# Performance work log

Measured on AMD Instinct MI355X. Metric: run time of the kernel, lower is better.

Reference implementation:

```python
import jax, jax.numpy as jnp
import numpy as np

B, C, N, T, Hd, L, F = 128, 8, 256, 64, 256, 2, 32  # batch, conv_channels, num_nodes(=hidden), obs_len, hidden, num_layers, filter_num


def setup_inputs() -> dict:
    key = jax.random.key(0)
    ks = jax.random.split(key, 20)
    s = 0.05
    f32 = jnp.float32
    return {
        "x": jax.random.normal(ks[0], (B, C, N, T), f32),
        "wst": jax.random.normal(ks[1], (C,), f32) * s,            # st_conv 1x1 weight
        "bst": jax.random.normal(ks[2], (1,), f32) * s,
        "Wh": jax.random.normal(ks[3], (Hd, N), f32) * s,           # hidden Linear
        "bh": jax.random.normal(ks[4], (Hd,), f32) * s,
        "Wih": jax.random.normal(ks[5], (4 * Hd, Hd), f32) * s,     # LSTM
        "Whh": jax.random.normal(ks[6], (4 * Hd, Hd), f32) * s,
        "bih": jax.random.normal(ks[7], (4 * Hd,), f32) * s,
        "bhh": jax.random.normal(ks[8], (4 * Hd,), f32) * s,
        "Wd": jax.random.normal(ks[9], (Hd, 2 * Hd), f32) * s,      # den Linear(2h->h)
        "bd": jax.random.normal(ks[10], (Hd,), f32) * s,
        "Wc": jax.random.normal(ks[11], (F, T), f32) * s,           # attention conv kernel (filter_num,1,obs_len,1) squeezed
        "bc": jax.random.normal(ks[12], (F,), f32) * s,
        "Wl1": jax.random.normal(ks[13], (F, 2 * Hd), f32) * s,     # attention linear1
        "bl1": jax.random.normal(ks[14], (F,), f32) * s,
        "Wl2": jax.random.normal(ks[15], (Hd, 2 * Hd + F), f32) * s,  # attention linear2
        "bl2": jax.random.normal(ks[16], (Hd,), f32) * s,
        "wend": jax.random.normal(ks[17], (C,), f32) * s,           # end_conv 1x1 weight
        "bend": jax.random.normal(ks[18], (C,), f32) * s,
    }


def _forward(x, wst, bst, Wh, bh, Wih, Whh, bih, bhh, Wd, bd, Wc, bc, Wl1, bl1, Wl2, bl2, wend, bend):
    b = x.shape[0]
    # st_conv (1x1 over channels) + relu, then (B, obs_len, num_nodes)
    y = jax.nn.relu(jnp.einsum("bcnt,c->bnt", x, wst) + bst[0])
    xcon = jax.nn.relu(jnp.einsum("bnt,hn->bth", y, Wh) + bh)  # (B, T, Hd)

    def lstm_cell(xt, ht, ct):
        g = xt @ Wih.T + bih + ht @ Whh.T + bhh
        i, f, gg, o = jnp.split(g, 4, axis=1)
        c2 = jax.nn.sigmoid(f) * ct + jax.nn.sigmoid(i) * jnp.tanh(gg)
        h2 = jax.nn.sigmoid(o) * jnp.tanh(c2)
        return h2, c2

    def attention(Hbuf, htt2):
        # Hbuf: (b, T, Hd); htt2: (b, 2Hd)
        w = htt2 @ Wl1.T + bl1                                   # (b, F)
        cv = jax.nn.relu(jnp.einsum("bto,ft->bof", Hbuf, Wc) + bc)  # (b, Hd, F)
        alpha = jax.nn.sigmoid(jnp.sum(cv * w[:, None, :], axis=2))  # (b, Hd)
        v = jnp.sum(alpha[:, :, None] * cv, axis=1)              # (b, F)
        return jax.nn.relu(jnp.concatenate([htt2, v], axis=1)) @ Wl2.T + bl2

    def step(carry, xt):
        ht, ct, attn_out, Hbuf = carry
        xi = xt
        new_ht = attn_out
        for _ in range(L):
            xd = jnp.concatenate([xi, attn_out], axis=1) @ Wd.T + bd
            ht, ct = lstm_cell(xd, ht, ct)
            htt2 = jnp.concatenate([ct, ht], axis=1)             # (b, 2Hd)
            new_ht = attention(Hbuf, htt2)                       # (b, Hd)
            output = jnp.concatenate([ht, new_ht], axis=1) @ Wd.T + bd
            Hbuf = jax.nn.relu(jnp.concatenate([Hbuf[:, 1:, :], output[:, None, :]], axis=1))
            attn_out = new_ht
            xi = output
        return (ht, ct, attn_out, Hbuf), new_ht

    z = jnp.zeros((b, Hd), x.dtype)
    carry0 = (z, z, z, jnp.zeros((b, T, Hd), x.dtype))
    _, res = jax.lax.scan(step, carry0, jnp.transpose(xcon, (1, 0, 2)))  # (T, b, Hd)
    r = jax.nn.relu(jnp.transpose(res, (1, 2, 0)))              # (b, Hd, T)
    # end_conv 1x1: (b, C, Hd, T)
    return r[:, None, :, :] * wend[None, :, None, None] + bend[None, :, None, None]


def reference(x, wst, bst, Wh, bh, Wih, Whh, bih, bhh, Wd, bd, Wc, bc, Wl1, bl1, Wl2, bl2, wend, bend):
    return _forward(x, wst, bst, Wh, bh, Wih, Whh, bih, bhh, Wd, bd, Wc, bc, Wl1, bl1, Wl2, bl2, wend, bend)
```

## Files before the change

kernel.cpp:

```cpp
#include <hip/hip_runtime.h>
#include <hip/hip_bf16.h>

typedef unsigned int uint;
typedef unsigned short ushort;
typedef __fp16 half2_t __attribute__((ext_vector_type(2)));

__device__ __forceinline__ ushort f16b(float x){
  return __builtin_bit_cast(ushort, (_Float16)x);
}
__device__ __forceinline__ uint pk_rne(float a, float b){
  return (uint)f16b(a) | ((uint)f16b(b) << 16);
}
__device__ __forceinline__ void pk_hl(float a, float b, uint& h, uint& l){
  _Float16 ha = (_Float16)a, hb = (_Float16)b;
  float la = (a - (float)ha) * 2048.f;
  float lb = (b - (float)hb) * 2048.f;
  h = (uint)__builtin_bit_cast(ushort, ha) | ((uint)__builtin_bit_cast(ushort, hb) << 16);
  l = pk_rne(la, lb);
}
__device__ __forceinline__ float fdot2(uint a, uint b, float c){
#if __has_builtin(__builtin_amdgcn_fdot2)
  return __builtin_amdgcn_fdot2(__builtin_bit_cast(half2_t, a),
                                __builtin_bit_cast(half2_t, b), c, false);
#else
  half2_t ha = __builtin_bit_cast(half2_t, a), hb = __builtin_bit_cast(half2_t, b);
  return c + (float)ha.x*(float)hb.x + (float)ha.y*(float)hb.y;
#endif
}
__device__ __forceinline__ float f16sel(uint p, uint hi){
  ushort us = hi ? (ushort)(p >> 16) : (ushort)(p & 0xffffu);
  return (float)__builtin_bit_cast(_Float16, us);
}
__device__ __forceinline__ float sigm(float x){ return 1.0f/(1.0f+__expf(-x)); }
__device__ __forceinline__ float tanh_(float x){
  x = fminf(fmaxf(x, -15.f), 15.f);
  float e = __expf(-2.f*x);
  return (1.f-e)/(1.f+e);
}
#define LO_SCALE (1.0f/2048.0f)


__global__ void kPack(const float* __restrict__ Wd, const float* __restrict__ Wih,
                      const float* __restrict__ Whh, const float* __restrict__ Wl1,
                      const float* __restrict__ Wl2, const float* __restrict__ Wc,
                      const float* __restrict__ Wh,  const float* __restrict__ bih,
                      const float* __restrict__ bhh,
                      uint4* __restrict__ Wd4, uint4* __restrict__ Wc4hi,
                      uint4* __restrict__ Wc4lo, uint4* __restrict__ Wl24,
                      float* __restrict__ Wl1f, uint* __restrict__ Wcrot,
                      uint* __restrict__ WhT2, float* __restrict__ bcomb)
{
  const int NTOT = 32768 + 65536 + 34816 + 16384 + 65536 + 32768 + 1024;
  for (int idx = blockIdx.x*blockDim.x + threadIdx.x; idx < NTOT; idx += gridDim.x*blockDim.x){
    int i = idx;
    if (i < 32768){
      int kpp=i>>8, o=i&255, k0=4*kpp;
      uint h0,l0,h1,l1;
      pk_hl(Wd[o*512+k0],   Wd[o*512+k0+1], h0,l0);
      pk_hl(Wd[o*512+k0+2], Wd[o*512+k0+3], h1,l1);
      Wd4[i] = make_uint4(h0,l0,h1,l1); continue; }
    i -= 32768;
    if (i < 65536){
      int kp=i>>8, hh=i&255;
      uint wh[4], wl[4];
      #pragma unroll
      for (int gi=0; gi<4; gi++){
        int row = gi*256+hh;
        float a,b;
        if (kp<128){ a=Wih[row*256+2*kp]; b=Wih[row*256+2*kp+1]; }
        else       { a=Whh[row*256+2*(kp-128)]; b=Whh[row*256+2*(kp-128)+1]; }
        pk_hl(a,b,wh[gi],wl[gi]);
      }
      Wc4hi[i] = make_uint4(wh[0],wh[1],wh[2],wh[3]);
      Wc4lo[i] = make_uint4(wl[0],wl[1],wl[2],wl[3]); continue; }
    i -= 65536;
    if (i < 34816){
      int kpp=i>>8, o=i&255, k0=4*kpp;
      uint h0,l0,h1,l1;
      pk_hl(Wl2[o*544+k0],   Wl2[o*544+k0+1], h0,l0);
      pk_hl(Wl2[o*544+k0+2], Wl2[o*544+k0+3], h1,l1);
      Wl24[i] = make_uint4(h0,l0,h1,l1); continue; }
    i -= 34816;
    if (i < 16384){ int kk=i>>5, f=i&31; Wl1f[i] = Wl1[f*512+kk]; continue; }
    i -= 16384;
    if (i < 65536){ int bb=i>>10, r=i&1023, ps=r>>5, f=r&31;
      float lo = Wc[f*64 + ((2*ps   - bb) & 63)];
      float hi = Wc[f*64 + ((2*ps+1 - bb) & 63)];
      Wcrot[i] = pk_rne(lo, hi); continue; }
    i -= 65536;
    if (i < 32768){ int np=i>>8, h=i&255;
      WhT2[i] = pk_rne(Wh[h*256+2*np], Wh[h*256+2*np+1]); continue; }
    i -= 32768;
    bcomb[i] = bih[i] + bhh[i];
  }
}

__global__ void k1a(const float* __restrict__ x, const float* __restrict__ wst,
                    const float* __restrict__ bst, ushort* __restrict__ yT)
{
  int b = blockIdx.x, tq = blockIdx.y, n = threadIdx.x;
  float acc[16];
  #pragma unroll
  for (int k=0;k<16;k++) acc[k]=0.f;
  for (int c=0;c<8;c++){
    const float4* xp = (const float4*)(x + ((size_t)((b*8+c)*256 + n)*64 + tq*16));
    float wc = wst[c];
    #pragma unroll
    for (int q=0;q<4;q++){
      float4 v = xp[q];
      acc[4*q+0] += v.x*wc; acc[4*q+1] += v.y*wc;
      acc[4*q+2] += v.z*wc; acc[4*q+3] += v.w*wc;
    }
  }
  float b0 = bst[0];
  #pragma unroll
  for (int k=0;k<16;k++){
    float v = fmaxf(acc[k]+b0, 0.f);
    yT[(size_t)(b*64 + tq*16 + k)*256 + n] = f16b(v);
  }
}

__global__ void k1b(const uint* __restrict__ yT2, const uint* __restrict__ WhT2,
                    const float* __restrict__ bh, float* __restrict__ xcon)
{
  __shared__ uint yp[8192];
  int b = blockIdx.x, tid = threadIdx.x;
  for (int i = tid; i < 8192; i += 256) yp[i] = yT2[(size_t)b*8192 + i];
  __syncthreads();
  int h = tid;
  float bias = bh[h];
  for (int tq=0;tq<4;tq++){
    float acc[16];
    #pragma unroll
    for (int k=0;k<16;k++) acc[k]=0.f;
    for (int np=0;np<128;np++){
      uint w2 = WhT2[np*256 + h];
      #pragma unroll
      for (int k=0;k<16;k++)
        acc[k] = fdot2(yp[(tq*16+k)*128 + np], w2, acc[k]);
    }
    #pragma unroll
    for (int k=0;k<16;k++)
      xcon[(size_t)(b*64 + tq*16 + k)*256 + h] = fmaxf(acc[k]+bias, 0.f);
  }
}

__global__ __launch_bounds__(1024, 1)
void TPALSTM_17205638987874_kernel(const float* __restrict__ xcon,
        const uint4* __restrict__ Wd4, const uint4* __restrict__ Wc4hi,
        const uint4* __restrict__ Wc4lo, const uint4* __restrict__ Wl24,
        const float* __restrict__ Wl1f, const uint* __restrict__ Wcrot,
        const float* __restrict__ bd, const float* __restrict__ bcomb,
        const float* __restrict__ bl1, const float* __restrict__ bl2,
        const float* __restrict__ bc, float* __restrict__ res)
{
  __shared__ uint  Hp[32][256];
  __shared__ uint  cvp[256][17];
  __shared__ float gp[16][256];
  __shared__ float p4[4][256];
  __shared__ float ht[256], ct[256], alpha[256];
  __shared__ __align__(16) uint2 APR2[288];
  __shared__ uint  wpair[16];

  int b = blockIdx.x, tid = threadIdx.x;
  int g = tid >> 8, o = tid & 255;

  for (int i = tid; i < 32*256; i += 1024) ((uint*)Hp)[i] = 0u;
  if (tid < 256){ ht[tid]=0.f; ct[tid]=0.f; }
  if (tid >= 128 && tid < 256) APR2[tid] = make_uint2(0u,0u);
  __syncthreads();

  int base = 0;
  for (int t=0;t<64;t++){
    if (tid < 128){
      const float* xr = xcon + (size_t)(b*64+t)*256;
      uint h,l; pk_hl(xr[2*tid], xr[2*tid+1], h, l);
      APR2[tid] = make_uint2(h,l);
    }
    __syncthreads();

    for (int l=0;l<2;l++){
      {
        float ahi=0.f, alo=0.f;
        const uint4* wp = Wd4 + (size_t)(g*32)*256 + o;
        const uint4* ap = (const uint4*)(APR2 + g*64);
        #pragma unroll 4
        for (int kpp=0;kpp<32;kpp++){
          uint4 w = wp[0]; wp += 256;
          uint4 A = ap[kpp];
          ahi = fdot2(A.x, w.x, ahi); alo = fdot2(A.y, w.x, alo); alo = fdot2(A.x, w.y, alo);
          ahi = fdot2(A.z, w.z, ahi); alo = fdot2(A.w, w.z, alo); alo = fdot2(A.z, w.w, alo);
        }
        p4[g][o] = ahi + alo*LO_SCALE;
      }
      __syncthreads();
      if (tid < 128){
        int o0=2*tid, o1=o0+1;
        float x0 = p4[0][o0]+p4[1][o0]+p4[2][o0]+p4[3][o0]+bd[o0];
        float x1 = p4[0][o1]+p4[1][o1]+p4[2][o1]+p4[3][o1]+bd[o1];
        uint h,l; pk_hl(x0,x1,h,l); APR2[tid]=make_uint2(h,l);
      } else if (tid < 256){
        int j=tid-128; uint h,l; pk_hl(ht[2*j], ht[2*j+1], h, l); APR2[tid]=make_uint2(h,l);
      }
      __syncthreads();
      {
        float ih=0.f,il=0.f,fh=0.f,fl=0.f,gh=0.f,gl=0.f,oh=0.f,ol=0.f;
        const uint4* whp = Wc4hi + (size_t)(g*64)*256 + o;
        const uint4* wlp = Wc4lo + (size_t)(g*64)*256 + o;
        #pragma unroll 2
        for (int kp=g*64; kp<g*64+64; kp++){
          uint4 w = whp[0]; whp += 256;
          uint4 v = wlp[0]; wlp += 256;
          uint2 A = APR2[kp];
          ih=fdot2(A.x,w.x,ih); il=fdot2(A.y,w.x,il); il=fdot2(A.x,v.x,il);
          fh=fdot2(A.x,w.y,fh); fl=fdot2(A.y,w.y,fl); fl=fdot2(A.x,v.y,fl);
          gh=fdot2(A.x,w.z,gh); gl=fdot2(A.y,w.z,gl); gl=fdot2(A.x,v.z,gl);
          oh=fdot2(A.x,w.w,oh); ol=fdot2(A.y,w.w,ol); ol=fdot2(A.x,v.w,ol);
        }
        gp[g*4+0][o]=ih+il*LO_SCALE; gp[g*4+1][o]=fh+fl*LO_SCALE;
        gp[g*4+2][o]=gh+gl*LO_SCALE; gp[g*4+3][o]=oh+ol*LO_SCALE;
      }
      __syncthreads();
      if (g==0){
        float gi = sigm (gp[0][o]+gp[4][o]+gp[8][o] +gp[12][o]+bcomb[o]);
        float gf = sigm (gp[1][o]+gp[5][o]+gp[9][o] +gp[13][o]+bcomb[256+o]);
        float gg = tanh_(gp[2][o]+gp[6][o]+gp[10][o]+gp[14][o]+bcomb[512+o]);
        float go = sigm (gp[3][o]+gp[7][o]+gp[11][o]+gp[15][o]+bcomb[768+o]);
        float c2 = gf*ct[o] + gi*gg;
        float h2 = go*tanh_(c2);
        ct[o]=c2; ht[o]=h2;
      }
      __syncthreads();
      if (tid < 128){ uint h,l; pk_hl(fmaxf(ct[2*tid],0.f), fmaxf(ct[2*tid+1],0.f), h,l); APR2[tid]=make_uint2(h,l); }
      else if (tid < 256){ int j=tid-128; uint h,l; pk_hl(fmaxf(ht[2*j],0.f), fmaxf(ht[2*j+1],0.f), h,l); APR2[tid]=make_uint2(h,l); }
      if (g==2 && o < 32){
        int f = o;
        float a=0.f;
        const float* w = Wl1f + f;
        for (int k=0;k<256;k++) a += ct[k]*w[k*32];
        for (int k=0;k<256;k++) a += ht[k]*w[(256+k)*32];
        float wtot = a + bl1[f];
        float wn = __shfl_xor(wtot,1);
        if (!(f&1)) wpair[f>>1] = pk_rne(wtot,wn);
      }
      if (g < 2){
        int rb = base & 63;
        const uint* wr = Wcrot + rb*1024 + g*16;
        float acc[16];
        #pragma unroll
        for (int j=0;j<16;j++) acc[j]=0.f;
        for (int ps=0;ps<32;ps++){
          uint hp = Hp[ps][o];
          const uint* w = wr + ps*32;
          #pragma unroll
          for (int j=0;j<16;j++) acc[j] = fdot2(hp, w[j], acc[j]);
        }
        #pragma unroll
        for (int jj=0;jj<8;jj++){
          int f0 = g*16 + 2*jj;
          cvp[o][g*8+jj] = pk_rne(fmaxf(acc[2*jj]+bc[f0],0.f),
                                  fmaxf(acc[2*jj+1]+bc[f0+1],0.f));
        }
      }
      __syncthreads();
      if (tid < 256){
        float s=0.f;
        #pragma unroll
        for (int p=0;p<16;p++) s = fdot2(cvp[tid][p], wpair[p], s);
        alpha[tid] = sigm(s);
      }
      __syncthreads();
      {
        int og = tid>>5, f = tid&31;
        uint hi = f&1; int fp=f>>1;
        float s=0.f;
        #pragma unroll
        for (int oo=0;oo<8;oo++){
          int oa = og*8+oo;
          s += alpha[oa]*f16sel(cvp[oa][fp], hi);
        }
        ((float*)gp)[og*32+f] = s;
      }
      __syncthreads();
      if (tid<32){
        float v=0.f;
        #pragma unroll
        for (int q=0;q<32;q++) v += ((float*)gp)[q*32+tid];
        float vn = __shfl_xor(v,1);
        if (!(tid&1)){
          uint h,l; pk_hl(fmaxf(v,0.f), fmaxf(vn,0.f), h,l);
          APR2[256+(tid>>1)]=make_uint2(h,l);
        }
      }
      __syncthreads();
      {
        float ahi=0.f, alo=0.f;
        const uint4* wp = Wl24 + (size_t)(g*34)*256 + o;
        const uint4* ap = (const uint4*)(APR2 + g*68);
        #pragma unroll 4
        for (int kpp=0;kpp<34;kpp++){
          uint4 w = wp[0]; wp += 256;
          uint4 A = ap[kpp];
          ahi = fdot2(A.x, w.x, ahi); alo = fdot2(A.y, w.x, alo); alo = fdot2(A.x, w.y, alo);
          ahi = fdot2(A.z, w.z, ahi); alo = fdot2(A.w, w.z, alo); alo = fdot2(A.z, w.w, alo);
        }
        p4[g][o] = ahi + alo*LO_SCALE;
      }
      __syncthreads();
      if (tid<128){ uint h,l; pk_hl(ht[2*tid], ht[2*tid+1], h,l); APR2[tid]=make_uint2(h,l); }
      else if (tid<256){
        int j=tid-128, o0=2*j, o1=o0+1;
        float n0 = p4[0][o0]+p4[1][o0]+p4[2][o0]+p4[3][o0]+bl2[o0];
        float n1 = p4[0][o1]+p4[1][o1]+p4[2][o1]+p4[3][o1]+bl2[o1];
        uint h,l; pk_hl(n0,n1,h,l); APR2[tid]=make_uint2(h,l);
        if (l==1){}
        if (1){
        }
        p4[0][o0] = n0; p4[0][o1] = n1;
      }
      __syncthreads();
      if (l==1 && tid>=128 && tid<256){
        int j=tid-128, o0=2*j, o1=o0+1;
        float* rr = res + (size_t)(t*128+b)*256;
        rr[o0] = p4[0][o0]; rr[o1] = p4[0][o1];
      }
      {
        float ahi=0.f, alo=0.f;
        const uint4* wp = Wd4 + (size_t)(g*32)*256 + o;
        const uint4* ap = (const uint4*)(APR2 + g*64);
        #pragma unroll 4
        for (int kpp=0;kpp<32;kpp++){
          uint4 w = wp[0]; wp += 256;
          uint4 A = ap[kpp];
          ahi = fdot2(A.x, w.x, ahi); alo = fdot2(A.y, w.x, alo); alo = fdot2(A.x, w.y, alo);
          ahi = fdot2(A.z, w.z, ahi); alo = fdot2(A.w, w.z, alo); alo = fdot2(A.z, w.w, alo);
        }
        __syncthreads();
        p4[g][o] = ahi + alo*LO_SCALE;
      }
      __syncthreads();
      if (tid<128){
        int o0=2*tid, o1=o0+1;
        float u0 = p4[0][o0]+p4[1][o0]+p4[2][o0]+p4[3][o0]+bd[o0];
        float u1 = p4[0][o1]+p4[1][o1]+p4[2][o1]+p4[3][o1]+bd[o1];
        uint h,l; pk_hl(u0, u1, h, l);
        APR2[tid]=make_uint2(h,l);
        int s = base & 63, ps = s>>1; uint hb = (uint)(s&1);
        uint h0 = (uint)f16b(fmaxf(u0,0.f)), h1 = (uint)f16b(fmaxf(u1,0.f));
        uint old0 = Hp[ps][o0], old1 = Hp[ps][o1];
        Hp[ps][o0] = hb ? ((old0&0xFFFFu)|(h0<<16)) : ((old0&0xFFFF0000u)|h0);
        Hp[ps][o1] = hb ? ((old1&0xFFFFu)|(h1<<16)) : ((old1&0xFFFF0000u)|h1);
      }
      __syncthreads();
      base++;
    }
  }
}

__global__ void k3(const float* __restrict__ res, const float* __restrict__ wend,
                   const float* __restrict__ bend, float* __restrict__ out)
{
  __shared__ float r2[64][257];
  int b = blockIdx.x, tid = threadIdx.x;
  for (int i = tid; i < 16384; i += 256){
    int t = i >> 8, h = i & 255;
    r2[t][h] = fmaxf(res[(size_t)(t*128+b)*256 + h], 0.f);
  }
  __syncthreads();
  int tt = tid & 63, hg = tid >> 6;
  for (int c=0;c<8;c++){
    float we = wend[c], be = bend[c];
    for (int hh=0;hh<64;hh++){
      int h = hg*64 + hh;
      out[((size_t)(b*8+c)*256 + h)*64 + tt] = r2[tt][h]*we + be;
    }
  }
}

extern "C" __attribute__((visibility("default"), used))
void kernel_launch(void* const* d_in, const int* in_sizes, int n_in,
                   void* d_out, int out_size, void* d_ws, size_t ws_size,
                   hipStream_t stream)
{
  const float* x    = (const float*)d_in[0];
  const float* wst  = (const float*)d_in[1];
  const float* bst  = (const float*)d_in[2];
  const float* Wh   = (const float*)d_in[3];
  const float* bh   = (const float*)d_in[4];
  const float* Wih  = (const float*)d_in[5];
  const float* Whh  = (const float*)d_in[6];
  const float* bih  = (const float*)d_in[7];
  const float* bhh  = (const float*)d_in[8];
  const float* Wd   = (const float*)d_in[9];
  const float* bd   = (const float*)d_in[10];
  const float* Wc   = (const float*)d_in[11];
  const float* bc   = (const float*)d_in[12];
  const float* Wl1  = (const float*)d_in[13];
  const float* bl1  = (const float*)d_in[14];
  const float* Wl2  = (const float*)d_in[15];
  const float* bl2  = (const float*)d_in[16];
  const float* wend = (const float*)d_in[17];
  const float* bend = (const float*)d_in[18];

  char* ws = (char*)d_ws;
  uint4* Wd4   = (uint4*)(ws + 0);
  uint4* Wc4hi = (uint4*)(ws + 524288);
  uint4* Wc4lo = (uint4*)(ws + 1572864);
  uint4* Wl24  = (uint4*)(ws + 2621440);
  float* Wl1f  = (float*)(ws + 3178496);
  uint*  Wcrot = (uint*) (ws + 3244032);
  uint*  WhT2  = (uint*) (ws + 3506176);
  float* bcomb = (float*)(ws + 3637248);
  ushort* yT   = (ushort*)(ws + 3641344);
  float* xcon  = (float*)(ws + 7835648);
  float* res   = (float*)(ws + 16224256);

  kPack<<<512, 256, 0, stream>>>(Wd, Wih, Whh, Wl1, Wl2, Wc, Wh, bih, bhh,
                                 Wd4, Wc4hi, Wc4lo, Wl24, Wl1f, Wcrot, WhT2, bcomb);
  k1a<<<dim3(128,4), 256, 0, stream>>>(x, wst, bst, yT);
  k1b<<<128, 256, 0, stream>>>((const uint*)yT, WhT2, bh, xcon);
  TPALSTM_17205638987874_kernel<<<128, 1024, 0, stream>>>(xcon, Wd4, Wc4hi, Wc4lo, Wl24,
                                                          Wl1f, Wcrot, bd, bcomb, bl1, bl2, bc, res);
  k3<<<128, 256, 0, stream>>>(res, wend, bend, (float*)d_out);
}
```

Before: 5.108 ms.

## Use hi/lo split fp16 for attention conv and spread it over all wave groups

The attention convolution now stores the history buffer and the rotated conv weights as a hi/lo fp16 pair and does three fdot2 per pair, which should give close to fp32 accuracy. The conv values are kept in fp32 shared memory rather than packed fp16. The conv work moves from two thread groups of 16 filters each to all four groups of 8 filters, and the Wl1 projection moves to group 3. This adds LDS traffic and extra dot products for accuracy, partly offset by the better spread of work across groups.

```diff
diff --git a/kernel.cpp b/kernel.cpp
--- a/kernel.cpp
+++ b/kernel.cpp
@@ -27,10 +27,6 @@
   return c + (float)ha.x*(float)hb.x + (float)ha.y*(float)hb.y;
 #endif
 }
-__device__ __forceinline__ float f16sel(uint p, uint hi){
-  ushort us = hi ? (ushort)(p >> 16) : (ushort)(p & 0xffffu);
-  return (float)__builtin_bit_cast(_Float16, us);
-}
 __device__ __forceinline__ float sigm(float x){ return 1.0f/(1.0f+__expf(-x)); }
 __device__ __forceinline__ float tanh_(float x){
   x = fminf(fmaxf(x, -15.f), 15.f);
@@ -47,8 +43,9 @@
                       const float* __restrict__ bhh,
                       uint4* __restrict__ Wd4, uint4* __restrict__ Wc4hi,
                       uint4* __restrict__ Wc4lo, uint4* __restrict__ Wl24,
-                      float* __restrict__ Wl1f, uint* __restrict__ Wcrot,
-                      uint* __restrict__ WhT2, float* __restrict__ bcomb)
+                      float* __restrict__ Wl1f, uint* __restrict__ WcrotH,
+                      uint* __restrict__ WcrotL, uint* __restrict__ WhT2,
+                      float* __restrict__ bcomb)
 {
   const int NTOT = 32768 + 65536 + 34816 + 16384 + 65536 + 32768 + 1024;
   for (int idx = blockIdx.x*blockDim.x + threadIdx.x; idx < NTOT; idx += gridDim.x*blockDim.x){
@@ -84,9 +81,10 @@
     if (i < 16384){ int kk=i>>5, f=i&31; Wl1f[i] = Wl1[f*512+kk]; continue; }
     i -= 16384;
     if (i < 65536){ int bb=i>>10, r=i&1023, ps=r>>5, f=r&31;
-      float lo = Wc[f*64 + ((2*ps   - bb) & 63)];
-      float hi = Wc[f*64 + ((2*ps+1 - bb) & 63)];
-      Wcrot[i] = pk_rne(lo, hi); continue; }
+      float va = Wc[f*64 + ((2*ps   - bb) & 63)];
+      float vb = Wc[f*64 + ((2*ps+1 - bb) & 63)];
+      uint h,l; pk_hl(va, vb, h, l);
+      WcrotH[i] = h; WcrotL[i] = l; continue; }
     i -= 65536;
     if (i < 32768){ int np=i>>8, h=i&255;
       WhT2[i] = pk_rne(Wh[h*256+2*np], Wh[h*256+2*np+1]); continue; }
@@ -149,23 +147,25 @@
 void TPALSTM_17205638987874_kernel(const float* __restrict__ xcon,
         const uint4* __restrict__ Wd4, const uint4* __restrict__ Wc4hi,
         const uint4* __restrict__ Wc4lo, const uint4* __restrict__ Wl24,
-        const float* __restrict__ Wl1f, const uint* __restrict__ Wcrot,
+        const float* __restrict__ Wl1f, const uint* __restrict__ WcrotH,
+        const uint* __restrict__ WcrotL,
         const float* __restrict__ bd, const float* __restrict__ bcomb,
         const float* __restrict__ bl1, const float* __restrict__ bl2,
         const float* __restrict__ bc, float* __restrict__ res)
 {
-  __shared__ uint  Hp[32][256];
-  __shared__ uint  cvp[256][17];
+  __shared__ uint  HpH[32][256];
+  __shared__ uint  HpL[32][256];
+  __shared__ float cvs[256][33];
   __shared__ float gp[16][256];
   __shared__ float p4[4][256];
   __shared__ float ht[256], ct[256], alpha[256];
   __shared__ __align__(16) uint2 APR2[288];
-  __shared__ uint  wpair[16];
+  __shared__ float wv[32];
 
   int b = blockIdx.x, tid = threadIdx.x;
   int g = tid >> 8, o = tid & 255;
 
-  for (int i = tid; i < 32*256; i += 1024) ((uint*)Hp)[i] = 0u;
+  for (int i = tid; i < 8192; i += 1024){ ((uint*)HpH)[i] = 0u; ((uint*)HpL)[i] = 0u; }
   if (tid < 256){ ht[tid]=0.f; ct[tid]=0.f; }
   if (tid >= 128 && tid < 256) APR2[tid] = make_uint2(0u,0u);
   __syncthreads();
@@ -233,51 +233,53 @@
       __syncthreads();
       if (tid < 128){ uint h,l; pk_hl(fmaxf(ct[2*tid],0.f), fmaxf(ct[2*tid+1],0.f), h,l); APR2[tid]=make_uint2(h,l); }
       else if (tid < 256){ int j=tid-128; uint h,l; pk_hl(fmaxf(ht[2*j],0.f), fmaxf(ht[2*j+1],0.f), h,l); APR2[tid]=make_uint2(h,l); }
-      if (g==2 && o < 32){
+      {
+        int rb = base & 63;
+        const uint* wrH = WcrotH + rb*1024 + g*8;
+        const uint* wrL = WcrotL + rb*1024 + g*8;
+        float ah[8], al[8];
+        #pragma unroll
+        for (int j=0;j<8;j++){ ah[j]=0.f; al[j]=0.f; }
+        for (int ps=0;ps<32;ps++){
+          uint hH = HpH[ps][o], hL = HpL[ps][o];
+          const uint* wH = wrH + ps*32;
+          const uint* wL = wrL + ps*32;
+          #pragma unroll
+          for (int j=0;j<8;j++){
+            ah[j] = fdot2(hH, wH[j], ah[j]);
+            al[j] = fdot2(hL, wH[j], al[j]);
+            al[j] = fdot2(hH, wL[j], al[j]);
+          }
+        }
+        #pragma unroll
+        for (int j=0;j<8;j++){
+          int f0 = g*8+j;
+          cvs[o][f0] = fmaxf(ah[j] + al[j]*LO_SCALE + bc[f0], 0.f);
+        }
+      }
+      if (g==3 && o < 32){
         int f = o;
         float a=0.f;
         const float* w = Wl1f + f;
         for (int k=0;k<256;k++) a += ct[k]*w[k*32];
         for (int k=0;k<256;k++) a += ht[k]*w[(256+k)*32];
-        float wtot = a + bl1[f];
-        float wn = __shfl_xor(wtot,1);
-        if (!(f&1)) wpair[f>>1] = pk_rne(wtot,wn);
-      }
-      if (g < 2){
-        int rb = base & 63;
-        const uint* wr = Wcrot + rb*1024 + g*16;
-        float acc[16];
-        #pragma unroll
-        for (int j=0;j<16;j++) acc[j]=0.f;
-        for (int ps=0;ps<32;ps++){
-          uint hp = Hp[ps][o];
-          const uint* w = wr + ps*32;
-          #pragma unroll
-          for (int j=0;j<16;j++) acc[j] = fdot2(hp, w[j], acc[j]);
-        }
-        #pragma unroll
-        for (int jj=0;jj<8;jj++){
-          int f0 = g*16 + 2*jj;
-          cvp[o][g*8+jj] = pk_rne(fmaxf(acc[2*jj]+bc[f0],0.f),
-                                  fmaxf(acc[2*jj+1]+bc[f0+1],0.f));
-        }
+        wv[f] = a + bl1[f];
       }
       __syncthreads();
       if (tid < 256){
         float s=0.f;
         #pragma unroll
-        for (int p=0;p<16;p++) s = fdot2(cvp[tid][p], wpair[p], s);
+        for (int f=0;f<32;f++) s += cvs[tid][f]*wv[f];
         alpha[tid] = sigm(s);
       }
       __syncthreads();
       {
         int og = tid>>5, f = tid&31;
-        uint hi = f&1; int fp=f>>1;
         float s=0.f;
         #pragma unroll
         for (int oo=0;oo<8;oo++){
           int oa = og*8+oo;
-          s += alpha[oa]*f16sel(cvp[oa][fp], hi);
+          s += alpha[oa]*cvs[oa][f];
         }
         ((float*)gp)[og*32+f] = s;
       }
@@ -313,9 +315,6 @@
         float n0 = p4[0][o0]+p4[1][o0]+p4[2][o0]+p4[3][o0]+bl2[o0];
         float n1 = p4[0][o1]+p4[1][o1]+p4[2][o1]+p4[3][o1]+bl2[o1];
         uint h,l; pk_hl(n0,n1,h,l); APR2[tid]=make_uint2(h,l);
-        if (l==1){}
-        if (1){
-        }
         p4[0][o0] = n0; p4[0][o1] = n1;
       }
       __syncthreads();
@@ -345,11 +344,19 @@
         float u1 = p4[0][o1]+p4[1][o1]+p4[2][o1]+p4[3][o1]+bd[o1];
         uint h,l; pk_hl(u0, u1, h, l);
         APR2[tid]=make_uint2(h,l);
+        float r0 = fmaxf(u0,0.f), r1 = fmaxf(u1,0.f);
+        _Float16 rh0 = (_Float16)r0, rh1 = (_Float16)r1;
+        uint h0 = (uint)__builtin_bit_cast(ushort, rh0);
+        uint h1 = (uint)__builtin_bit_cast(ushort, rh1);
+        uint l0 = (uint)f16b((r0-(float)rh0)*2048.f);
+        uint l1 = (uint)f16b((r1-(float)rh1)*2048.f);
         int s = base & 63, ps = s>>1; uint hb = (uint)(s&1);
-        uint h0 = (uint)f16b(fmaxf(u0,0.f)), h1 = (uint)f16b(fmaxf(u1,0.f));
-        uint old0 = Hp[ps][o0], old1 = Hp[ps][o1];
-        Hp[ps][o0] = hb ? ((old0&0xFFFFu)|(h0<<16)) : ((old0&0xFFFF0000u)|h0);
-        Hp[ps][o1] = hb ? ((old1&0xFFFFu)|(h1<<16)) : ((old1&0xFFFF0000u)|h1);
+        uint oldH0 = HpH[ps][o0], oldH1 = HpH[ps][o1];
+        uint oldL0 = HpL[ps][o0], oldL1 = HpL[ps][o1];
+        HpH[ps][o0] = hb ? ((oldH0&0xFFFFu)|(h0<<16)) : ((oldH0&0xFFFF0000u)|h0);
+        HpH[ps][o1] = hb ? ((oldH1&0xFFFFu)|(h1<<16)) : ((oldH1&0xFFFF0000u)|h1);
+        HpL[ps][o0] = hb ? ((oldL0&0xFFFFu)|(l0<<16)) : ((oldL0&0xFFFF0000u)|l0);
+        HpL[ps][o1] = hb ? ((oldL1&0xFFFFu)|(l1<<16)) : ((oldL1&0xFFFF0000u)|l1);
       }
       __syncthreads();
       base++;
@@ -403,23 +410,25 @@
   const float* bend = (const float*)d_in[18];
 
   char* ws = (char*)d_ws;
-  uint4* Wd4   = (uint4*)(ws + 0);
-  uint4* Wc4hi = (uint4*)(ws + 524288);
-  uint4* Wc4lo = (uint4*)(ws + 1572864);
-  uint4* Wl24  = (uint4*)(ws + 2621440);
-  float* Wl1f  = (float*)(ws + 3178496);
-  uint*  Wcrot = (uint*) (ws + 3244032);
-  uint*  WhT2  = (uint*) (ws + 3506176);
-  float* bcomb = (float*)(ws + 3637248);
-  ushort* yT   = (ushort*)(ws + 3641344);
-  float* xcon  = (float*)(ws + 7835648);
-  float* res   = (float*)(ws + 16224256);
+  uint4* Wd4    = (uint4*)(ws + 0);
+  uint4* Wc4hi  = (uint4*)(ws + 524288);
+  uint4* Wc4lo  = (uint4*)(ws + 1572864);
+  uint4* Wl24   = (uint4*)(ws + 2621440);
+  float* Wl1f   = (float*)(ws + 3178496);
+  uint*  WcrotH = (uint*) (ws + 3244032);
+  uint*  WcrotL = (uint*) (ws + 3506176);
+  uint*  WhT2   = (uint*) (ws + 3768320);
+  float* bcomb  = (float*)(ws + 3899392);
+  ushort* yT    = (ushort*)(ws + 3903488);
+  float* xcon   = (float*)(ws + 8097792);
+  float* res    = (float*)(ws + 16486400);
 
   kPack<<<512, 256, 0, stream>>>(Wd, Wih, Whh, Wl1, Wl2, Wc, Wh, bih, bhh,
-                                 Wd4, Wc4hi, Wc4lo, Wl24, Wl1f, Wcrot, WhT2, bcomb);
+                                 Wd4, Wc4hi, Wc4lo, Wl24, Wl1f, WcrotH, WcrotL, WhT2, bcomb);
   k1a<<<dim3(128,4), 256, 0, stream>>>(x, wst, bst, yT);
   k1b<<<128, 256, 0, stream>>>((const uint*)yT, WhT2, bh, xcon);
   TPALSTM_17205638987874_kernel<<<128, 1024, 0, stream>>>(xcon, Wd4, Wc4hi, Wc4lo, Wl24,
-                                                          Wl1f, Wcrot, bd, bcomb, bl1, bl2, bc, res);
+                                                          Wl1f, WcrotH, WcrotL,
+                                                          bd, bcomb, bl1, bl2, bc, res);
   k3<<<128, 256, 0, stream>>>(res, wend, bend, (float*)d_out);
 }
```

Measured after the change: 6.423 ms. +25.7%, slower.
